# Performance work log

Measured on AMD Instinct MI355X. Metric: run time of the kernel, lower is better.

## Reference

```python
import jax, jax.numpy as jnp
import numpy as np

STATE_DIM = 128
NUM_STATES = 16
BATCH = 16384


def setup_inputs() -> dict:
    key = jax.random.key(0)
    k1, k2, k3, k4 = jax.random.split(key, 4)
    x = jax.random.normal(k1, (BATCH, STATE_DIM), dtype=jnp.float32)
    state_idx = jax.random.randint(k2, (BATCH,), 0, NUM_STATES)
    A_all = jax.random.normal(k3, (NUM_STATES, STATE_DIM, STATE_DIM), dtype=jnp.float32)
    C_all = jax.random.normal(k4, (NUM_STATES, STATE_DIM, STATE_DIM), dtype=jnp.float32)
    return {"x": x, "state_idx": state_idx, "A_all": A_all, "C_all": C_all}


def reference(x, state_idx, A_all, C_all):
    # Per-sample expert matrix gather: [B, D, D]
    Ag = A_all[state_idx]
    Cg = C_all[state_idx]
    # state = relu(x @ A_i) per sample, batched via einsum
    state = jax.nn.relu(jnp.einsum('bd,bde->be', x, Ag))
    # observation = state @ C_i
    out = jnp.einsum('be,bef->bf', state, Cg)
    return out
```

## Files before the change

kernel.cpp:

```cpp
#include <hip/hip_runtime.h>

#define D 128
#define NS 16
#define BATCH 16384
#define TILE 64
#define CHUNK 512

typedef __attribute__((ext_vector_type(8))) short short8;
typedef __attribute__((ext_vector_type(4))) float f32x4;

__device__ __forceinline__ unsigned short f2bf(float f) {
  unsigned u = __builtin_bit_cast(unsigned, f);
  u += 0x7FFFu + ((u >> 16) & 1u);
  return (unsigned short)(u >> 16);
}

__device__ __forceinline__ uint4 pack8(float4 a, float4 b) {
  unsigned short p[8];
  p[0] = f2bf(a.x); p[1] = f2bf(a.y); p[2] = f2bf(a.z); p[3] = f2bf(a.w);
  p[4] = f2bf(b.x); p[5] = f2bf(b.y); p[6] = f2bf(b.z); p[7] = f2bf(b.w);
  return *(const uint4*)p;
}

__global__ __launch_bounds__(256, 2) void ssm_fused(
    const float* __restrict__ x,
    const int* __restrict__ sidx,
    const float* __restrict__ A_all,
    const float* __restrict__ C_all,
    float* __restrict__ out) {
  __shared__ unsigned short XH[TILE * D];
  __shared__ int rowlist[CHUNK];
  __shared__ int wcnt[8];

  const int b = blockIdx.x;
  const int s = (b & 7) | (((b >> 3) & 1) << 3);
  const int c0 = (b >> 4) * CHUNK;
  const int tid = threadIdx.x;
  const int lane = tid & 63, w = tid >> 6;
  const int l15 = lane & 15, quad = lane >> 4;

  const int v0 = sidx[c0 + tid];
  const int v1 = sidx[c0 + 256 + tid];

  short8 aW[4][2], cW[4][2];
  {
    const size_t wb = (size_t)s * D * D;
    const int col = w * 32 + l15;
#pragma unroll
    for (int kb = 0; kb < 4; kb++)
#pragma unroll
      for (int nb = 0; nb < 2; nb++) {
        const float* pA =
            A_all + wb + (size_t)(kb * 32 + quad * 8) * D + col + nb * 16;
        const float* pC =
            C_all + wb + (size_t)(kb * 32 + quad * 8) * D + col + nb * 16;
        unsigned short ta[8], tc[8];
#pragma unroll
        for (int j = 0; j < 8; j++) {
          ta[j] = f2bf(pA[j * D]);
          tc[j] = f2bf(pC[j * D]);
        }
        aW[kb][nb] = *(const short8*)ta;
        cW[kb][nb] = *(const short8*)tc;
      }
  }

  const unsigned long long lanelt = (1ull << lane) - 1ull;
  const unsigned long long m0 = __ballot(v0 == s);
  const unsigned long long m1 = __ballot(v1 == s);
  if (lane == 0) { wcnt[w] = (int)__popcll(m0); wcnt[4 + w] = (int)__popcll(m1); }
  __syncthreads();
  int pre0 = 0, pre1 = 0, tot0 = 0, cnt = 0;
#pragma unroll
  for (int ww = 0; ww < 4; ww++) {
    if (ww < w) { pre0 += wcnt[ww]; pre1 += wcnt[4 + ww]; }
    tot0 += wcnt[ww];
    cnt += wcnt[ww] + wcnt[4 + ww];
  }
  if (v0 == s) rowlist[pre0 + (int)__popcll(m0 & lanelt)] = c0 + tid;
  if (v1 == s) rowlist[tot0 + pre1 + (int)__popcll(m1 & lanelt)] = c0 + 256 + tid;
  if (cnt == 0) return;

#pragma unroll 1
  for (int i0 = 0; i0 < cnt; i0 += TILE) {
    __syncthreads();

    {
      const int r = tid >> 2, q = tid & 3;
      const int rid = (i0 + r < cnt) ? rowlist[i0 + r] : -1;
      if (rid >= 0) {
        const float4* src = (const float4*)(x + (size_t)rid * D + q * 32);
#pragma unroll
        for (int i = 0; i < 4; i++) {
          float4 va = src[2 * i];
          float4 vb = src[2 * i + 1];
          *(uint4*)&XH[r * D + (((q * 4 + i) ^ (r & 15)) << 3)] = pack8(va, vb);
        }
      } else {
        uint4 z = {0, 0, 0, 0};
#pragma unroll
        for (int i = 0; i < 4; i++)
          *(uint4*)&XH[r * D + (((q * 4 + i) ^ (r & 15)) << 3)] = z;
      }
    }
    __syncthreads();

    f32x4 acc[4][2];
#pragma unroll
    for (int ti = 0; ti < 4; ti++) {
      acc[ti][0] = (f32x4){0.f, 0.f, 0.f, 0.f};
      acc[ti][1] = (f32x4){0.f, 0.f, 0.f, 0.f};
    }
#pragma unroll
    for (int kb = 0; kb < 4; kb++) {
      short8 aF[4];
#pragma unroll
      for (int ti = 0; ti < 4; ti++)
        aF[ti] = *(const short8*)&XH[(ti * 16 + l15) * D +
                                     (((kb * 4 + quad) ^ l15) << 3)];
#pragma unroll
      for (int ti = 0; ti < 4; ti++) {
        acc[ti][0] = __builtin_amdgcn_mfma_f32_16x16x32_bf16(aF[ti], aW[kb][0],
                                                             acc[ti][0], 0, 0, 0);
        acc[ti][1] = __builtin_amdgcn_mfma_f32_16x16x32_bf16(aF[ti], aW[kb][1],
                                                             acc[ti][1], 0, 0, 0);
      }
    }
    __syncthreads();

#pragma unroll
    for (int ti = 0; ti < 4; ti++)
#pragma unroll
      for (int nb = 0; nb < 2; nb++)
#pragma unroll
        for (int rr = 0; rr < 4; rr++) {
          float v = acc[ti][nb][rr];
          const int row = ti * 16 + quad * 4 + rr;
          const int ch = (w * 4 + nb * 2 + (l15 >> 3)) ^ (quad * 4 + rr);
          XH[row * D + (ch << 3) + (l15 & 7)] = f2bf(v > 0.f ? v : 0.f);
        }
    __syncthreads();

#pragma unroll
    for (int ti = 0; ti < 4; ti++) {
      acc[ti][0] = (f32x4){0.f, 0.f, 0.f, 0.f};
      acc[ti][1] = (f32x4){0.f, 0.f, 0.f, 0.f};
    }
#pragma unroll
    for (int kb = 0; kb < 4; kb++) {
      short8 aF[4];
#pragma unroll
      for (int ti = 0; ti < 4; ti++)
        aF[ti] = *(const short8*)&XH[(ti * 16 + l15) * D +
                                     (((kb * 4 + quad) ^ l15) << 3)];
#pragma unroll
      for (int ti = 0; ti < 4; ti++) {
        acc[ti][0] = __builtin_amdgcn_mfma_f32_16x16x32_bf16(aF[ti], cW[kb][0],
                                                             acc[ti][0], 0, 0, 0);
        acc[ti][1] = __builtin_amdgcn_mfma_f32_16x16x32_bf16(aF[ti], cW[kb][1],
                                                             acc[ti][1], 0, 0, 0);
      }
    }

#pragma unroll
    for (int ti = 0; ti < 4; ti++)
#pragma unroll
      for (int rr = 0; rr < 4; rr++) {
        const int rl = i0 + ti * 16 + quad * 4 + rr;
        if (rl < cnt) {
          float* orow = out + (size_t)rowlist[rl] * D + w * 32 + l15;
          orow[0] = acc[ti][0][rr];
          orow[16] = acc[ti][1][rr];
        }
      }
  }
}

extern "C" void kernel_launch(void* const* d_in, const int* in_sizes, int n_in,
                              void* d_out, int out_size, void* d_ws, size_t ws_size,
                              hipStream_t stream) {
  const float* x = (const float*)d_in[0];
  const int* sidx = (const int*)d_in[1];
  const float* A_all = (const float*)d_in[2];
  const float* C_all = (const float*)d_in[3];
  float* out = (float*)d_out;

  ssm_fused<<<512, 256, 0, stream>>>(x, sidx, A_all, C_all, out);
}
```

Before: 71.92 us.

## Double per-block row chunk and skip empty 16-row subtiles in MFMA loops

Each block now scans 1024 batch rows for its expert state instead of 512, which halves the grid to 256 blocks and halves how often each block converts the per-state A and C weights to bf16 registers. Inside the tile loop, 16-row subtiles that lie beyond the gathered row count now skip their LDS fragment loads, MFMAs, ReLU write-back and stores. With about 64 matching rows per block, most blocks process about one full tile plus a partial one. The cost is fewer blocks in flight on the GPU and extra branch logic in the inner loops.

```diff
diff --git a/kernel.cpp b/kernel.cpp
--- a/kernel.cpp
+++ b/kernel.cpp
@@ -4,7 +4,7 @@
 #define NS 16
 #define BATCH 16384
 #define TILE 64
-#define CHUNK 512
+#define CHUNK 1024
 
 typedef __attribute__((ext_vector_type(8))) short short8;
 typedef __attribute__((ext_vector_type(4))) float f32x4;
@@ -30,10 +30,10 @@
     float* __restrict__ out) {
   __shared__ unsigned short XH[TILE * D];
   __shared__ int rowlist[CHUNK];
-  __shared__ int wcnt[8];
+  __shared__ int wcnt[16];
 
   const int b = blockIdx.x;
-  const int s = (b & 7) | (((b >> 3) & 1) << 3);
+  const int s = b & 15;
   const int c0 = (b >> 4) * CHUNK;
   const int tid = threadIdx.x;
   const int lane = tid & 63, w = tid >> 6;
@@ -41,6 +41,8 @@
 
   const int v0 = sidx[c0 + tid];
   const int v1 = sidx[c0 + 256 + tid];
+  const int v2 = sidx[c0 + 512 + tid];
+  const int v3 = sidx[c0 + 768 + tid];
 
   short8 aW[4][2], cW[4][2];
   {
@@ -68,22 +70,39 @@
   const unsigned long long lanelt = (1ull << lane) - 1ull;
   const unsigned long long m0 = __ballot(v0 == s);
   const unsigned long long m1 = __ballot(v1 == s);
-  if (lane == 0) { wcnt[w] = (int)__popcll(m0); wcnt[4 + w] = (int)__popcll(m1); }
+  const unsigned long long m2 = __ballot(v2 == s);
+  const unsigned long long m3 = __ballot(v3 == s);
+  if (lane == 0) {
+    wcnt[w] = (int)__popcll(m0);
+    wcnt[4 + w] = (int)__popcll(m1);
+    wcnt[8 + w] = (int)__popcll(m2);
+    wcnt[12 + w] = (int)__popcll(m3);
+  }
   __syncthreads();
-  int pre0 = 0, pre1 = 0, tot0 = 0, cnt = 0;
-#pragma unroll
-  for (int ww = 0; ww < 4; ww++) {
-    if (ww < w) { pre0 += wcnt[ww]; pre1 += wcnt[4 + ww]; }
-    tot0 += wcnt[ww];
-    cnt += wcnt[ww] + wcnt[4 + ww];
-  }
-  if (v0 == s) rowlist[pre0 + (int)__popcll(m0 & lanelt)] = c0 + tid;
-  if (v1 == s) rowlist[tot0 + pre1 + (int)__popcll(m1 & lanelt)] = c0 + 256 + tid;
+  int preg[4], cnt = 0;
+#pragma unroll
+  for (int g = 0; g < 4; g++) {
+    preg[g] = cnt;
+    int sub = 0;
+#pragma unroll
+    for (int ww = 0; ww < 4; ww++) {
+      const int c = wcnt[g * 4 + ww];
+      if (ww < w) sub += c;
+      cnt += c;
+    }
+    preg[g] += sub;
+  }
+  if (v0 == s) rowlist[preg[0] + (int)__popcll(m0 & lanelt)] = c0 + tid;
+  if (v1 == s) rowlist[preg[1] + (int)__popcll(m1 & lanelt)] = c0 + 256 + tid;
+  if (v2 == s) rowlist[preg[2] + (int)__popcll(m2 & lanelt)] = c0 + 512 + tid;
+  if (v3 == s) rowlist[preg[3] + (int)__popcll(m3 & lanelt)] = c0 + 768 + tid;
   if (cnt == 0) return;
 
 #pragma unroll 1
   for (int i0 = 0; i0 < cnt; i0 += TILE) {
     __syncthreads();
+
+    const bool tv1 = (i0 + 16 < cnt), tv2 = (i0 + 32 < cnt), tv3 = (i0 + 48 < cnt);
 
     {
       const int r = tid >> 2, q = tid & 3;
@@ -115,11 +134,18 @@
     for (int kb = 0; kb < 4; kb++) {
       short8 aF[4];
 #pragma unroll
-      for (int ti = 0; ti < 4; ti++)
+      for (int ti = 0; ti < 4; ti++) {
+        if (ti == 1 && !tv1) continue;
+        if (ti == 2 && !tv2) continue;
+        if (ti == 3 && !tv3) continue;
         aF[ti] = *(const short8*)&XH[(ti * 16 + l15) * D +
                                      (((kb * 4 + quad) ^ l15) << 3)];
-#pragma unroll
-      for (int ti = 0; ti < 4; ti++) {
+      }
+#pragma unroll
+      for (int ti = 0; ti < 4; ti++) {
+        if (ti == 1 && !tv1) continue;
+        if (ti == 2 && !tv2) continue;
+        if (ti == 3 && !tv3) continue;
         acc[ti][0] = __builtin_amdgcn_mfma_f32_16x16x32_bf16(aF[ti], aW[kb][0],
                                                              acc[ti][0], 0, 0, 0);
         acc[ti][1] = __builtin_amdgcn_mfma_f32_16x16x32_bf16(aF[ti], aW[kb][1],
@@ -129,7 +155,10 @@
     __syncthreads();
 
 #pragma unroll
-    for (int ti = 0; ti < 4; ti++)
+    for (int ti = 0; ti < 4; ti++) {
+      if (ti == 1 && !tv1) continue;
+      if (ti == 2 && !tv2) continue;
+      if (ti == 3 && !tv3) continue;
 #pragma unroll
       for (int nb = 0; nb < 2; nb++)
 #pragma unroll
@@ -139,6 +168,7 @@
           const int ch = (w * 4 + nb * 2 + (l15 >> 3)) ^ (quad * 4 + rr);
           XH[row * D + (ch << 3) + (l15 & 7)] = f2bf(v > 0.f ? v : 0.f);
         }
+    }
     __syncthreads();
 
 #pragma unroll
@@ -150,11 +180,18 @@
     for (int kb = 0; kb < 4; kb++) {
       short8 aF[4];
 #pragma unroll
-      for (int ti = 0; ti < 4; ti++)
+      for (int ti = 0; ti < 4; ti++) {
+        if (ti == 1 && !tv1) continue;
+        if (ti == 2 && !tv2) continue;
+        if (ti == 3 && !tv3) continue;
         aF[ti] = *(const short8*)&XH[(ti * 16 + l15) * D +
                                      (((kb * 4 + quad) ^ l15) << 3)];
-#pragma unroll
-      for (int ti = 0; ti < 4; ti++) {
+      }
+#pragma unroll
+      for (int ti = 0; ti < 4; ti++) {
+        if (ti == 1 && !tv1) continue;
+        if (ti == 2 && !tv2) continue;
+        if (ti == 3 && !tv3) continue;
         acc[ti][0] = __builtin_amdgcn_mfma_f32_16x16x32_bf16(aF[ti], cW[kb][0],
                                                              acc[ti][0], 0, 0, 0);
         acc[ti][1] = __builtin_amdgcn_mfma_f32_16x16x32_bf16(aF[ti], cW[kb][1],
@@ -163,7 +200,10 @@
     }
 
 #pragma unroll
-    for (int ti = 0; ti < 4; ti++)
+    for (int ti = 0; ti < 4; ti++) {
+      if (ti == 1 && !tv1) continue;
+      if (ti == 2 && !tv2) continue;
+      if (ti == 3 && !tv3) continue;
 #pragma unroll
       for (int rr = 0; rr < 4; rr++) {
         const int rl = i0 + ti * 16 + quad * 4 + rr;
@@ -173,6 +213,7 @@
           orow[16] = acc[ti][1][rr];
         }
       }
+    }
   }
 }
 
@@ -185,5 +226,5 @@
   const float* C_all = (const float*)d_in[3];
   float* out = (float*)d_out;
 
-  ssm_fused<<<512, 256, 0, stream>>>(x, sidx, A_all, C_all, out);
-}
+  ssm_fused<<<BATCH / CHUNK * NS, 256, 0, stream>>>(x, sidx, A_all, C_all, out);
+}
```

Result: no change. 73.10 us (+1.6%).

## Use 512-thread blocks with 8 waves each owning 16 output columns

Applied to the files above, without the earlier changes.

Doubles the block size to 512 threads so each of 8 waves computes a 16-column slice instead of 4 waves with 32 columns. Each thread now scans one index instead of two, and per-thread weight registers and accumulators are halved. The aim is more waves in flight to hide latency during the gather, MFMA and store phases. In exchange there are more waves per block contending at the barriers, and per-wave MFMA work per barrier is smaller.

```diff
diff --git a/kernel.cpp b/kernel.cpp
--- a/kernel.cpp
+++ b/kernel.cpp
@@ -22,7 +22,7 @@
   return *(const uint4*)p;
 }
 
-__global__ __launch_bounds__(256, 2) void ssm_fused(
+__global__ __launch_bounds__(512, 4) void ssm_fused(
     const float* __restrict__ x,
     const int* __restrict__ sidx,
     const float* __restrict__ A_all,
@@ -40,45 +40,38 @@
   const int l15 = lane & 15, quad = lane >> 4;
 
   const int v0 = sidx[c0 + tid];
-  const int v1 = sidx[c0 + 256 + tid];
 
-  short8 aW[4][2], cW[4][2];
+  short8 aW[4], cW[4];
   {
     const size_t wb = (size_t)s * D * D;
-    const int col = w * 32 + l15;
+    const int col = w * 16 + l15;
 #pragma unroll
-    for (int kb = 0; kb < 4; kb++)
+    for (int kb = 0; kb < 4; kb++) {
+      const float* pA = A_all + wb + (size_t)(kb * 32 + quad * 8) * D + col;
+      const float* pC = C_all + wb + (size_t)(kb * 32 + quad * 8) * D + col;
+      unsigned short ta[8], tc[8];
 #pragma unroll
-      for (int nb = 0; nb < 2; nb++) {
-        const float* pA =
-            A_all + wb + (size_t)(kb * 32 + quad * 8) * D + col + nb * 16;
-        const float* pC =
-            C_all + wb + (size_t)(kb * 32 + quad * 8) * D + col + nb * 16;
-        unsigned short ta[8], tc[8];
-#pragma unroll
-        for (int j = 0; j < 8; j++) {
-          ta[j] = f2bf(pA[j * D]);
-          tc[j] = f2bf(pC[j * D]);
-        }
-        aW[kb][nb] = *(const short8*)ta;
-        cW[kb][nb] = *(const short8*)tc;
+      for (int j = 0; j < 8; j++) {
+        ta[j] = f2bf(pA[j * D]);
+        tc[j] = f2bf(pC[j * D]);
       }
+      aW[kb] = *(const short8*)ta;
+      cW[kb] = *(const short8*)tc;
+    }
   }
 
   const unsigned long long lanelt = (1ull << lane) - 1ull;
   const unsigned long long m0 = __ballot(v0 == s);
-  const unsigned long long m1 = __ballot(v1 == s);
-  if (lane == 0) { wcnt[w] = (int)__popcll(m0); wcnt[4 + w] = (int)__popcll(m1); }
+  if (lane == 0) wcnt[w] = (int)__popcll(m0);
   __syncthreads();
-  int pre0 = 0, pre1 = 0, tot0 = 0, cnt = 0;
+  int pre = 0, cnt = 0;
 #pragma unroll
-  for (int ww = 0; ww < 4; ww++) {
-    if (ww < w) { pre0 += wcnt[ww]; pre1 += wcnt[4 + ww]; }
-    tot0 += wcnt[ww];
-    cnt += wcnt[ww] + wcnt[4 + ww];
+  for (int ww = 0; ww < 8; ww++) {
+    const int c = wcnt[ww];
+    if (ww < w) pre += c;
+    cnt += c;
   }
-  if (v0 == s) rowlist[pre0 + (int)__popcll(m0 & lanelt)] = c0 + tid;
-  if (v1 == s) rowlist[tot0 + pre1 + (int)__popcll(m1 & lanelt)] = c0 + 256 + tid;
+  if (v0 == s) rowlist[pre + (int)__popcll(m0 & lanelt)] = c0 + tid;
   if (cnt == 0) return;
 
 #pragma unroll 1
@@ -86,31 +79,26 @@
     __syncthreads();
 
     {
-      const int r = tid >> 2, q = tid & 3;
+      const int r = tid >> 3, q8 = tid & 7;
       const int rid = (i0 + r < cnt) ? rowlist[i0 + r] : -1;
+      const int cA = q8 * 2, cB = q8 * 2 + 1;
+      uint4* dA = (uint4*)&XH[r * D + ((cA ^ (r & 15)) << 3)];
+      uint4* dB = (uint4*)&XH[r * D + ((cB ^ (r & 15)) << 3)];
       if (rid >= 0) {
-        const float4* src = (const float4*)(x + (size_t)rid * D + q * 32);
-#pragma unroll
-        for (int i = 0; i < 4; i++) {
-          float4 va = src[2 * i];
-          float4 vb = src[2 * i + 1];
-          *(uint4*)&XH[r * D + (((q * 4 + i) ^ (r & 15)) << 3)] = pack8(va, vb);
-        }
+        const float4* src = (const float4*)(x + (size_t)rid * D + q8 * 16);
+        *dA = pack8(src[0], src[1]);
+        *dB = pack8(src[2], src[3]);
       } else {
         uint4 z = {0, 0, 0, 0};
-#pragma unroll
-        for (int i = 0; i < 4; i++)
-          *(uint4*)&XH[r * D + (((q * 4 + i) ^ (r & 15)) << 3)] = z;
+        *dA = z;
+        *dB = z;
       }
     }
     __syncthreads();
 
-    f32x4 acc[4][2];
+    f32x4 acc[4];
 #pragma unroll
-    for (int ti = 0; ti < 4; ti++) {
-      acc[ti][0] = (f32x4){0.f, 0.f, 0.f, 0.f};
-      acc[ti][1] = (f32x4){0.f, 0.f, 0.f, 0.f};
-    }
+    for (int ti = 0; ti < 4; ti++) acc[ti] = (f32x4){0.f, 0.f, 0.f, 0.f};
 #pragma unroll
     for (int kb = 0; kb < 4; kb++) {
       short8 aF[4];
@@ -119,33 +107,25 @@
         aF[ti] = *(const short8*)&XH[(ti * 16 + l15) * D +
                                      (((kb * 4 + quad) ^ l15) << 3)];
 #pragma unroll
-      for (int ti = 0; ti < 4; ti++) {
-        acc[ti][0] = __builtin_amdgcn_mfma_f32_16x16x32_bf16(aF[ti], aW[kb][0],
-                                                             acc[ti][0], 0, 0, 0);
-        acc[ti][1] = __builtin_amdgcn_mfma_f32_16x16x32_bf16(aF[ti], aW[kb][1],
-                                                             acc[ti][1], 0, 0, 0);
-      }
+      for (int ti = 0; ti < 4; ti++)
+        acc[ti] = __builtin_amdgcn_mfma_f32_16x16x32_bf16(aF[ti], aW[kb],
+                                                          acc[ti], 0, 0, 0);
     }
     __syncthreads();
 
 #pragma unroll
     for (int ti = 0; ti < 4; ti++)
 #pragma unroll
-      for (int nb = 0; nb < 2; nb++)
-#pragma unroll
-        for (int rr = 0; rr < 4; rr++) {
-          float v = acc[ti][nb][rr];
-          const int row = ti * 16 + quad * 4 + rr;
-          const int ch = (w * 4 + nb * 2 + (l15 >> 3)) ^ (quad * 4 + rr);
-          XH[row * D + (ch << 3) + (l15 & 7)] = f2bf(v > 0.f ? v : 0.f);
-        }
+      for (int rr = 0; rr < 4; rr++) {
+        float v = acc[ti][rr];
+        const int row = ti * 16 + quad * 4 + rr;
+        const int ch = (w * 2 + (l15 >> 3)) ^ (quad * 4 + rr);
+        XH[row * D + (ch << 3) + (l15 & 7)] = f2bf(v > 0.f ? v : 0.f);
+      }
     __syncthreads();
 
 #pragma unroll
-    for (int ti = 0; ti < 4; ti++) {
-      acc[ti][0] = (f32x4){0.f, 0.f, 0.f, 0.f};
-      acc[ti][1] = (f32x4){0.f, 0.f, 0.f, 0.f};
-    }
+    for (int ti = 0; ti < 4; ti++) acc[ti] = (f32x4){0.f, 0.f, 0.f, 0.f};
 #pragma unroll
     for (int kb = 0; kb < 4; kb++) {
       short8 aF[4];
@@ -154,12 +134,9 @@
         aF[ti] = *(const short8*)&XH[(ti * 16 + l15) * D +
                                      (((kb * 4 + quad) ^ l15) << 3)];
 #pragma unroll
-      for (int ti = 0; ti < 4; ti++) {
-        acc[ti][0] = __builtin_amdgcn_mfma_f32_16x16x32_bf16(aF[ti], cW[kb][0],
-                                                             acc[ti][0], 0, 0, 0);
-        acc[ti][1] = __builtin_amdgcn_mfma_f32_16x16x32_bf16(aF[ti], cW[kb][1],
-                                                             acc[ti][1], 0, 0, 0);
-      }
+      for (int ti = 0; ti < 4; ti++)
+        acc[ti] = __builtin_amdgcn_mfma_f32_16x16x32_bf16(aF[ti], cW[kb],
+                                                          acc[ti], 0, 0, 0);
     }
 
 #pragma unroll
@@ -168,9 +145,7 @@
       for (int rr = 0; rr < 4; rr++) {
         const int rl = i0 + ti * 16 + quad * 4 + rr;
         if (rl < cnt) {
-          float* orow = out + (size_t)rowlist[rl] * D + w * 32 + l15;
-          orow[0] = acc[ti][0][rr];
-          orow[16] = acc[ti][1][rr];
+          out[(size_t)rowlist[rl] * D + w * 16 + l15] = acc[ti][rr];
         }
       }
   }
@@ -185,5 +160,5 @@
   const float* C_all = (const float*)d_in[3];
   float* out = (float*)d_out;
 
-  ssm_fused<<<512, 256, 0, stream>>>(x, sidx, A_all, C_all, out);
+  ssm_fused<<<BATCH / CHUNK * NS, 512, 0, stream>>>(x, sidx, A_all, C_all, out);
 }
```

Result: no change. 71.65 us (-0.4%).
